# Optimization experiments

Measured on AMD Instinct MI355X. Metric: run time of the kernel, lower is better.

Reference implementation:

```python
import jax, jax.numpy as jnp
import numpy as np

N, DEG, F, H, O, B = 100000, 16, 128, 128, 128, 8192


def setup_inputs() -> dict:
    key = jax.random.key(0)
    k1, k2, k3, k4, k5 = jax.random.split(key, 5)
    features = jax.random.normal(k1, (N, F), dtype=jnp.float32)
    w1 = jax.random.normal(k2, (2 * F, H), dtype=jnp.float32)
    w2 = jax.random.normal(k3, (2 * H, O), dtype=jnp.float32)
    neighbor_idx = jax.random.randint(k4, (N, DEG), 0, N, dtype=jnp.int32)
    nodes = jax.random.randint(k5, (B,), 0, N, dtype=jnp.int32)
    return {"features": features, "w1": w1, "w2": w2,
            "neighbor_idx": neighbor_idx, "nodes": nodes}


def reference(features, w1, w2, neighbor_idx, nodes):
    # Layer 1 (computed for all nodes, vectorized): mean-aggregate neighbor
    # raw features, concat with self features, project with w1.
    neigh_feat = features[neighbor_idx]                 # [N, DEG, F] gather
    agg1 = neigh_feat.mean(axis=1)                      # [N, F]
    h1 = jnp.concatenate([features, agg1], axis=-1) @ w1  # [N, H]

    # Layer 2 (batch nodes): mean-aggregate neighbor layer-1 embeddings,
    # concat with self layer-1 embedding, project with w2.
    h1_self = h1[nodes]                                 # [B, H]
    h1_neigh = h1[neighbor_idx[nodes]].mean(axis=1)     # [B, H]
    out = jnp.concatenate([h1_self, h1_neigh], axis=-1) @ w2  # [B, O]
    return out
```

## Files before the change

kernel.cpp:

```cpp
#include <hip/hip_runtime.h>


#define N_NODES 100000
#define DEG     16
#define FDIM    128
#define HDIM    128
#define B_NODES 8192

typedef __attribute__((ext_vector_type(8))) short bf16x8;
typedef __attribute__((ext_vector_type(8))) unsigned short u16x8;
typedef __attribute__((ext_vector_type(4))) float f32x4;
typedef __attribute__((ext_vector_type(2))) float f32x2;

static __device__ __forceinline__ unsigned short f2bf(float f) {
    union { float f; unsigned u; } v; v.f = f;
    unsigned r = v.u + 0x7fff + ((v.u >> 16) & 1);
    return (unsigned short)(r >> 16);
}
static __device__ __forceinline__ float bf2f(unsigned short b) {
    union { unsigned u; float f; } v; v.u = ((unsigned)b) << 16;
    return v.f;
}

__global__ __launch_bounds__(256)
void prep(const float* __restrict__ feat, const float* __restrict__ w1,
          const float* __restrict__ w2, unsigned short* __restrict__ fb,
          unsigned char* __restrict__ f8,
          unsigned short* __restrict__ w1T, unsigned short* __restrict__ w2T) {
    if (blockIdx.x < 6250) {
        long e = ((long)blockIdx.x * 256 + threadIdx.x) * 8;
        float4 v0 = *(const float4*)(feat + e);
        float4 v1 = *(const float4*)(feat + e + 4);
        u16x8 ob;
        ob[0] = f2bf(v0.x); ob[1] = f2bf(v0.y); ob[2] = f2bf(v0.z); ob[3] = f2bf(v0.w);
        ob[4] = f2bf(v1.x); ob[5] = f2bf(v1.y); ob[6] = f2bf(v1.z); ob[7] = f2bf(v1.w);
        *(u16x8*)(fb + e) = ob;
        int p0 = 0, p1 = 0;
        p0 = __builtin_amdgcn_cvt_pk_fp8_f32(v0.x, v0.y, p0, false);
        p0 = __builtin_amdgcn_cvt_pk_fp8_f32(v0.z, v0.w, p0, true);
        p1 = __builtin_amdgcn_cvt_pk_fp8_f32(v1.x, v1.y, p1, false);
        p1 = __builtin_amdgcn_cvt_pk_fp8_f32(v1.z, v1.w, p1, true);
        uint2 o8; o8.x = (unsigned)p0; o8.y = (unsigned)p1;
        *(uint2*)(f8 + e) = o8;
    } else {
        int bid = blockIdx.x - 6250;
        const float* w = (bid < 8) ? w1 : w2;
        unsigned short* wT = (bid < 8) ? w1T : w2T;
        int kb = (bid & 7) * 32;
        int n = threadIdx.x & 127, dk = threadIdx.x >> 7;
#pragma unroll
        for (int i = 0; i < 16; ++i) {
            int k = kb + dk * 16 + i;
            wT[n * 256 + k] = f2bf(w[k * 128 + n]);
        }
    }
}

__global__ __launch_bounds__(64)
void k1_agg(const unsigned char* __restrict__ f8, const int* __restrict__ nbr,
            unsigned short* __restrict__ agg) {
    __shared__ unsigned char L[8][1024];
    const int lane = threadIdx.x;
    const int node = blockIdx.x * 8 + (lane >> 3);
    const int sub = lane & 7;
    const int* idx = nbr + node * DEG;
    int4 i0 = *(const int4*)(idx);
    int4 i1 = *(const int4*)(idx + 4);
    int4 i2 = *(const int4*)(idx + 8);
    int4 i3 = *(const int4*)(idx + 12);
    const int id[16] = {i0.x, i0.y, i0.z, i0.w, i1.x, i1.y, i1.z, i1.w,
                        i2.x, i2.y, i2.z, i2.w, i3.x, i3.y, i3.z, i3.w};

#define K1_ISSUE(Q, B)                                                          \
    _Pragma("unroll")                                                           \
    for (int j_ = 0; j_ < 4; ++j_) {                                            \
        const unsigned char* src_ = f8 + (long)id[(Q) * 4 + j_] * 128 + sub * 16; \
        __builtin_amdgcn_global_load_lds(                                       \
            (const __attribute__((address_space(1))) unsigned int*)src_,        \
            (__attribute__((address_space(3))) unsigned int*)                   \
                (&L[(B) * 4 + j_][lane * 16]), 16, 0, 0);                       \
    }

    f32x2 s2[8];
#pragma unroll
    for (int j = 0; j < 8; ++j) s2[j] = (f32x2){0.f, 0.f};

#define K1_CONV(B)                                                              \
    _Pragma("unroll")                                                           \
    for (int j_ = 0; j_ < 4; ++j_) {                                            \
        uint4 v = *(const uint4*)(&L[(B) * 4 + j_][lane * 16]);                 \
        s2[0] += __builtin_amdgcn_cvt_pk_f32_fp8((int)v.x, false);              \
        s2[1] += __builtin_amdgcn_cvt_pk_f32_fp8((int)v.x, true);               \
        s2[2] += __builtin_amdgcn_cvt_pk_f32_fp8((int)v.y, false);              \
        s2[3] += __builtin_amdgcn_cvt_pk_f32_fp8((int)v.y, true);               \
        s2[4] += __builtin_amdgcn_cvt_pk_f32_fp8((int)v.z, false);              \
        s2[5] += __builtin_amdgcn_cvt_pk_f32_fp8((int)v.z, true);               \
        s2[6] += __builtin_amdgcn_cvt_pk_f32_fp8((int)v.w, false);              \
        s2[7] += __builtin_amdgcn_cvt_pk_f32_fp8((int)v.w, true);               \
    }

    K1_ISSUE(0, 0);
    K1_ISSUE(1, 1);
    asm volatile("s_waitcnt vmcnt(4)" ::: "memory");
    __builtin_amdgcn_sched_barrier(0);
    K1_CONV(0);
    __builtin_amdgcn_sched_barrier(0);
    K1_ISSUE(2, 0);
    asm volatile("s_waitcnt vmcnt(4)" ::: "memory");
    __builtin_amdgcn_sched_barrier(0);
    K1_CONV(1);
    __builtin_amdgcn_sched_barrier(0);
    K1_ISSUE(3, 1);
    asm volatile("s_waitcnt vmcnt(4)" ::: "memory");
    __builtin_amdgcn_sched_barrier(0);
    K1_CONV(0);
    asm volatile("s_waitcnt vmcnt(0)" ::: "memory");
    __builtin_amdgcn_sched_barrier(0);
    K1_CONV(1);

    u16x8 o0, o1;
#pragma unroll
    for (int j = 0; j < 8; ++j) {
        o0[j] = f2bf(s2[j >> 1][j & 1] * 0.0625f);
        o1[j] = f2bf(s2[4 + (j >> 1)][j & 1] * 0.0625f);
    }
    unsigned short* dst = agg + (long)node * 128 + sub * 16;
    *(u16x8*)dst = o0;
    *(u16x8*)(dst + 8) = o1;
}

#define STAGE8(KC)                                                                            \
    do {                                                                                      \
        const unsigned short* s0_ = ((KC) < 4) ? (fb + (KC) * 32) : (agg + ((KC) - 4) * 32);  \
        _Pragma("unroll")                                                                     \
        for (int j_ = 0; j_ < 2; ++j_) {                                                      \
            long grow_ = row0 + (t >> 2) + j_ * 64;                                           \
            const unsigned short* ga_ = s0_ + grow_ * 128 + (t & 3) * 8;                      \
            __builtin_amdgcn_global_load_lds(                                                 \
                (const __attribute__((address_space(1))) unsigned int*)ga_,                   \
                (__attribute__((address_space(3))) unsigned int*)                             \
                    (&AsS[(KC) * 4096 + wave * 512 + j_ * 2048 + lane * 8]), 16, 0, 0);       \
            const unsigned short* gw_ = w1T + ((t >> 2) + j_ * 64) * 256 + (KC) * 32 + (t & 3) * 8; \
            __builtin_amdgcn_global_load_lds(                                                 \
                (const __attribute__((address_space(1))) unsigned int*)gw_,                   \
                (__attribute__((address_space(3))) unsigned int*)                             \
                    (&WsS[(KC) * 4096 + wave * 512 + j_ * 2048 + lane * 8]), 16, 0, 0);       \
        }                                                                                     \
    } while (0)

__global__ __launch_bounds__(256)
void g1(const unsigned short* __restrict__ fb, const unsigned short* __restrict__ agg,
        const unsigned short* __restrict__ w1T, unsigned short* __restrict__ h1) {
    __shared__ unsigned short AsS[8 * 4096];
    __shared__ unsigned short WsS[8 * 4096];
    const int t = threadIdx.x, wave = t >> 6, lane = t & 63;
    const int m16 = lane & 15, quad = lane >> 4;
    const long row0 = (long)blockIdx.x * 128;

    STAGE8(0); STAGE8(1); STAGE8(2); STAGE8(3);
    STAGE8(4); STAGE8(5); STAGE8(6); STAGE8(7);
    __syncthreads();

    f32x4 acc[2][8] = {};
#pragma unroll
    for (int kc = 0; kc < 8; ++kc) {
        const unsigned short* Ab = &AsS[kc * 4096];
        const unsigned short* Wb = &WsS[kc * 4096];
        bf16x8 a0 = *(const bf16x8*)(Ab + (wave * 32 + m16) * 32 + quad * 8);
        bf16x8 a1 = *(const bf16x8*)(Ab + (wave * 32 + 16 + m16) * 32 + quad * 8);
#pragma unroll
        for (int nt = 0; nt < 8; ++nt) {
            bf16x8 bv = *(const bf16x8*)(Wb + (nt * 16 + m16) * 32 + quad * 8);
            acc[0][nt] = __builtin_amdgcn_mfma_f32_16x16x32_bf16(a0, bv, acc[0][nt], 0, 0, 0);
            acc[1][nt] = __builtin_amdgcn_mfma_f32_16x16x32_bf16(a1, bv, acc[1][nt], 0, 0, 0);
        }
    }

#pragma unroll
    for (int mt = 0; mt < 2; ++mt)
#pragma unroll
        for (int reg = 0; reg < 4; ++reg) {
            long grow = row0 + wave * 32 + mt * 16 + quad * 4 + reg;
            if (grow >= N_NODES) continue;
#pragma unroll
            for (int nt = 0; nt < 8; ++nt)
                h1[grow * HDIM + nt * 16 + m16] = f2bf(acc[mt][nt][reg]);
        }
}

__global__ __launch_bounds__(256)
void g2_fused(const unsigned short* __restrict__ h1, const unsigned short* __restrict__ w2T,
              const int* __restrict__ nbr, const int* __restrict__ nodes,
              float* __restrict__ out) {
    __shared__ unsigned short X2[64][264];
    const int t = threadIdx.x, wave = t >> 6, lane = t & 63;
    const int m16 = lane & 15, quad = lane >> 4;
    const int b0 = blockIdx.x * 64;
    const int colb = m16 * 8;

    for (int g = 0; g < 4; ++g) {
        int Ln = wave * 16 + g * 4 + quad;
        int node = nodes[b0 + Ln];
        *(u16x8*)(&X2[Ln][colb]) = *(const u16x8*)(h1 + (long)node * HDIM + colb);
        const int* idx = nbr + node * DEG;
        int4 i0 = *(const int4*)(idx);
        int4 i1 = *(const int4*)(idx + 4);
        int4 i2 = *(const int4*)(idx + 8);
        int4 i3 = *(const int4*)(idx + 12);
        const int id[16] = {i0.x, i0.y, i0.z, i0.w, i1.x, i1.y, i1.z, i1.w,
                            i2.x, i2.y, i2.z, i2.w, i3.x, i3.y, i3.z, i3.w};

        uint4 v0, v1, v2, v3, v4, v5, v6, v7, v8, v9, v10, v11, v12, v13, v14, v15;
#define G2_LOAD(K)                                                               \
        {                                                                        \
            unsigned long long a_ =                                              \
                (unsigned long long)(h1 + (long)id[K] * HDIM + colb);            \
            asm volatile("global_load_dwordx4 %0, %1, off"                       \
                         : "=v"(v##K) : "v"(a_) : "memory");                     \
        }
        G2_LOAD(0)  G2_LOAD(1)  G2_LOAD(2)  G2_LOAD(3)
        G2_LOAD(4)  G2_LOAD(5)  G2_LOAD(6)  G2_LOAD(7)
        G2_LOAD(8)  G2_LOAD(9)  G2_LOAD(10) G2_LOAD(11)
        G2_LOAD(12) G2_LOAD(13) G2_LOAD(14) G2_LOAD(15)
#undef G2_LOAD

        float s[8] = {0.f, 0.f, 0.f, 0.f, 0.f, 0.f, 0.f, 0.f};
        asm volatile("s_waitcnt vmcnt(8)" ::: "memory");
        __builtin_amdgcn_sched_barrier(0);
#define G2_SUM(K)                                                                \
        {                                                                        \
            u16x8 w_ = __builtin_bit_cast(u16x8, v##K);                          \
            _Pragma("unroll")                                                    \
            for (int j = 0; j < 8; ++j) s[j] += bf2f(w_[j]);                     \
        }
        G2_SUM(0) G2_SUM(1) G2_SUM(2) G2_SUM(3)
        G2_SUM(4) G2_SUM(5) G2_SUM(6) G2_SUM(7)
        asm volatile("s_waitcnt vmcnt(0)" ::: "memory");
        __builtin_amdgcn_sched_barrier(0);
        G2_SUM(8)  G2_SUM(9)  G2_SUM(10) G2_SUM(11)
        G2_SUM(12) G2_SUM(13) G2_SUM(14) G2_SUM(15)
#undef G2_SUM

        u16x8 o;
#pragma unroll
        for (int j = 0; j < 8; ++j) o[j] = f2bf(s[j] * 0.0625f);
        *(u16x8*)(&X2[Ln][128 + colb]) = o;
    }
    __syncthreads();

    f32x4 acc[8] = {};
#pragma unroll
    for (int kc = 0; kc < 8; ++kc) {
        bf16x8 a = *(const bf16x8*)(&X2[wave * 16 + m16][kc * 32 + quad * 8]);
#pragma unroll
        for (int nt = 0; nt < 8; ++nt) {
            bf16x8 b = *(const bf16x8*)(w2T + (nt * 16 + m16) * 256 + kc * 32 + quad * 8);
            acc[nt] = __builtin_amdgcn_mfma_f32_16x16x32_bf16(a, b, acc[nt], 0, 0, 0);
        }
    }

#pragma unroll
    for (int nt = 0; nt < 8; ++nt)
#pragma unroll
        for (int reg = 0; reg < 4; ++reg) {
            int row = b0 + wave * 16 + quad * 4 + reg;
            out[(long)row * 128 + nt * 16 + m16] = acc[nt][reg];
        }
}

extern "C" void kernel_launch(void* const* d_in, const int* in_sizes, int n_in,
                              void* d_out, int out_size, void* d_ws, size_t ws_size,
                              hipStream_t stream) {
    const float* feat  = (const float*)d_in[0];
    const float* w1    = (const float*)d_in[1];
    const float* w2    = (const float*)d_in[2];
    const int*   nbr   = (const int*)d_in[3];
    const int*   nodes = (const int*)d_in[4];
    float* out = (float*)d_out;

    char* ws = (char*)d_ws;
    unsigned short* fb  = (unsigned short*)ws;
    unsigned char*  f8  = (unsigned char*)(ws + 25600000);
    unsigned short* agg = (unsigned short*)(ws + 38400000);
    unsigned short* h1  = (unsigned short*)(ws + 64000000);
    unsigned short* w1T = (unsigned short*)(ws + 89600000);
    unsigned short* w2T = (unsigned short*)(ws + 89665536);

    prep<<<6266, 256, 0, stream>>>(feat, w1, w2, fb, f8, w1T, w2T);
    k1_agg<<<12500, 64, 0, stream>>>(f8, nbr, agg);
    g1<<<(N_NODES + 127) / 128, 256, 0, stream>>>(fb, agg, w1T, h1);
    g2_fused<<<B_NODES / 64, 256, 0, stream>>>(h1, w2T, nbr, nodes, out);
}
```

Measured before the change: 172.6 us.

## Load g1 A operands directly into registers, stage only W1 in LDS

The g1 GEMM kernel no longer stages the activation tile through LDS. Each wave now loads its A fragments (features and aggregated rows) straight into VGPRs with inline global_load_dwordx4, and only w1T is staged in LDS, pre-laid out in MFMA fragment order. This halves LDS usage to allow two blocks per CU (launch_bounds 256,2) and removes the LDS reads for A. In exchange it raises register pressure (16 uint4 held live) and uses a less coalesced row-strided global access pattern for A.

```diff
diff --git a/kernel.cpp b/kernel.cpp
--- a/kernel.cpp
+++ b/kernel.cpp
@@ -129,58 +129,81 @@
     *(u16x8*)(dst + 8) = o1;
 }
 
-#define STAGE8(KC)                                                                            \
-    do {                                                                                      \
-        const unsigned short* s0_ = ((KC) < 4) ? (fb + (KC) * 32) : (agg + ((KC) - 4) * 32);  \
-        _Pragma("unroll")                                                                     \
-        for (int j_ = 0; j_ < 2; ++j_) {                                                      \
-            long grow_ = row0 + (t >> 2) + j_ * 64;                                           \
-            const unsigned short* ga_ = s0_ + grow_ * 128 + (t & 3) * 8;                      \
-            __builtin_amdgcn_global_load_lds(                                                 \
-                (const __attribute__((address_space(1))) unsigned int*)ga_,                   \
-                (__attribute__((address_space(3))) unsigned int*)                             \
-                    (&AsS[(KC) * 4096 + wave * 512 + j_ * 2048 + lane * 8]), 16, 0, 0);       \
-            const unsigned short* gw_ = w1T + ((t >> 2) + j_ * 64) * 256 + (KC) * 32 + (t & 3) * 8; \
-            __builtin_amdgcn_global_load_lds(                                                 \
-                (const __attribute__((address_space(1))) unsigned int*)gw_,                   \
-                (__attribute__((address_space(3))) unsigned int*)                             \
-                    (&WsS[(KC) * 4096 + wave * 512 + j_ * 2048 + lane * 8]), 16, 0, 0);       \
-        }                                                                                     \
-    } while (0)
-
-__global__ __launch_bounds__(256)
+__global__ __launch_bounds__(256, 2)
 void g1(const unsigned short* __restrict__ fb, const unsigned short* __restrict__ agg,
         const unsigned short* __restrict__ w1T, unsigned short* __restrict__ h1) {
-    __shared__ unsigned short AsS[8 * 4096];
-    __shared__ unsigned short WsS[8 * 4096];
+    __shared__ unsigned short Wlds[64 * 512];
     const int t = threadIdx.x, wave = t >> 6, lane = t & 63;
     const int m16 = lane & 15, quad = lane >> 4;
-    const long row0 = (long)blockIdx.x * 128;
-
-    STAGE8(0); STAGE8(1); STAGE8(2); STAGE8(3);
-    STAGE8(4); STAGE8(5); STAGE8(6); STAGE8(7);
+    const long row0 = (long)blockIdx.x * 128 + wave * 32;
+
+    uint4 a0_0, a0_1, a1_0, a1_1, a2_0, a2_1, a3_0, a3_1;
+    uint4 a4_0, a4_1, a5_0, a5_1, a6_0, a6_1, a7_0, a7_1;
+#define G1_LOAD(KC, MT, V)                                                       \
+    {                                                                            \
+        const unsigned short* As_ =                                              \
+            ((KC) < 4) ? (fb + (KC) * 32) : (agg + ((KC) - 4) * 32);             \
+        unsigned long long ad_ =                                                 \
+            (unsigned long long)(As_ + (row0 + (MT) * 16 + m16) * 128 + quad * 8); \
+        asm volatile("global_load_dwordx4 %0, %1, off"                           \
+                     : "=v"(V) : "v"(ad_) : "memory");                           \
+    }
+    G1_LOAD(0, 0, a0_0) G1_LOAD(0, 1, a0_1)
+    G1_LOAD(1, 0, a1_0) G1_LOAD(1, 1, a1_1)
+    G1_LOAD(2, 0, a2_0) G1_LOAD(2, 1, a2_1)
+    G1_LOAD(3, 0, a3_0) G1_LOAD(3, 1, a3_1)
+    G1_LOAD(4, 0, a4_0) G1_LOAD(4, 1, a4_1)
+    G1_LOAD(5, 0, a5_0) G1_LOAD(5, 1, a5_1)
+    G1_LOAD(6, 0, a6_0) G1_LOAD(6, 1, a6_1)
+    G1_LOAD(7, 0, a7_0) G1_LOAD(7, 1, a7_1)
+#undef G1_LOAD
+
+#pragma unroll
+    for (int i = 0; i < 16; ++i) {
+        int o16 = i * 256 + t;
+        int chunk = o16 >> 6;
+        int kc = chunk >> 3, nt = chunk & 7;
+        int n = nt * 16 + m16;
+        int k0 = kc * 32 + quad * 8;
+        const unsigned short* src = w1T + n * 256 + k0;
+        __builtin_amdgcn_global_load_lds(
+            (const __attribute__((address_space(1))) unsigned int*)src,
+            (__attribute__((address_space(3))) unsigned int*)
+                (((char*)Wlds) + (long)o16 * 16),
+            16, 0, 0);
+    }
+
+    asm volatile("s_waitcnt vmcnt(0)" ::: "memory");
+    __builtin_amdgcn_sched_barrier(0);
     __syncthreads();
 
     f32x4 acc[2][8] = {};
-#pragma unroll
-    for (int kc = 0; kc < 8; ++kc) {
-        const unsigned short* Ab = &AsS[kc * 4096];
-        const unsigned short* Wb = &WsS[kc * 4096];
-        bf16x8 a0 = *(const bf16x8*)(Ab + (wave * 32 + m16) * 32 + quad * 8);
-        bf16x8 a1 = *(const bf16x8*)(Ab + (wave * 32 + 16 + m16) * 32 + quad * 8);
-#pragma unroll
-        for (int nt = 0; nt < 8; ++nt) {
-            bf16x8 bv = *(const bf16x8*)(Wb + (nt * 16 + m16) * 32 + quad * 8);
-            acc[0][nt] = __builtin_amdgcn_mfma_f32_16x16x32_bf16(a0, bv, acc[0][nt], 0, 0, 0);
-            acc[1][nt] = __builtin_amdgcn_mfma_f32_16x16x32_bf16(a1, bv, acc[1][nt], 0, 0, 0);
-        }
-    }
+#define G1_KC(KC, V0, V1)                                                        \
+    {                                                                            \
+        bf16x8 a0 = __builtin_bit_cast(bf16x8, V0);                              \
+        bf16x8 a1 = __builtin_bit_cast(bf16x8, V1);                              \
+        _Pragma("unroll")                                                        \
+        for (int nt = 0; nt < 8; ++nt) {                                         \
+            bf16x8 bv = *(const bf16x8*)(Wlds + ((KC) * 8 + nt) * 512 + lane * 8); \
+            acc[0][nt] = __builtin_amdgcn_mfma_f32_16x16x32_bf16(a0, bv, acc[0][nt], 0, 0, 0); \
+            acc[1][nt] = __builtin_amdgcn_mfma_f32_16x16x32_bf16(a1, bv, acc[1][nt], 0, 0, 0); \
+        }                                                                        \
+    }
+    G1_KC(0, a0_0, a0_1)
+    G1_KC(1, a1_0, a1_1)
+    G1_KC(2, a2_0, a2_1)
+    G1_KC(3, a3_0, a3_1)
+    G1_KC(4, a4_0, a4_1)
+    G1_KC(5, a5_0, a5_1)
+    G1_KC(6, a6_0, a6_1)
+    G1_KC(7, a7_0, a7_1)
+#undef G1_KC
 
 #pragma unroll
     for (int mt = 0; mt < 2; ++mt)
 #pragma unroll
         for (int reg = 0; reg < 4; ++reg) {
-            long grow = row0 + wave * 32 + mt * 16 + quad * 4 + reg;
+            long grow = row0 + mt * 16 + quad * 4 + reg;
             if (grow >= N_NODES) continue;
 #pragma unroll
             for (int nt = 0; nt < 8; ++nt)
```

After: 172.7 us. About the same (+0.1%).
